# Performance work log

Hardware: AMD Instinct MI355X
Metric: run time of the kernel (lower is better)

Reference implementation:

```python
import jax, jax.numpy as jnp
import numpy as np

T, B, L, S = 2048, 64, 32, 256
NEG = -1e30  # effective -inf, safe under logaddexp


def setup_inputs() -> dict:
    key = jax.random.key(0)
    k1, k2, k3 = jax.random.split(key, 3)
    inputs = jax.random.normal(k1, (T, B, L), dtype=jnp.float32)
    targets = jax.random.randint(k2, (B, S), 0, L)
    input_lengths = jnp.full((B,), T, dtype=jnp.int32)
    target_lengths = jnp.full((B,), S, dtype=jnp.int32)
    # learned transition matrix (param of ASGLoss); small random for a non-trivial test
    transition = 0.1 * jax.random.normal(k3, (L, L), dtype=jnp.float32)
    return {"transition": transition, "inputs": inputs, "targets": targets,
            "input_lengths": input_lengths, "target_lengths": target_lengths}


def _fcc_scores(transition, inputs, input_lengths):
    # Fully-connected forward: alpha_t[i] = emit_t[i] + logsumexp_j(alpha_{t-1}[j] + trans[i,j])
    alpha0 = inputs[0]  # [B, L]

    def step(alpha, emit):
        new = emit + jax.nn.logsumexp(alpha[:, None, :] + transition[None, :, :], axis=2)
        return new, new

    _, rest = jax.lax.scan(step, alpha0, inputs[1:])
    alphas = jnp.concatenate([alpha0[None], rest], axis=0)  # [T, B, L]
    b = jnp.arange(inputs.shape[1])
    # causal DP: alpha at t = len-1 is exactly the score for that length
    return jax.nn.logsumexp(alphas[input_lengths - 1, b], axis=-1)  # [B]


def _fac_scores(transition, inputs, targets, input_lengths, target_lengths):
    # Force-aligned forward over target positions s:
    # alpha_t[s] = emit_t[tgt_s] + logaddexp(alpha_{t-1}[s] + trans[tgt_s,tgt_s],
    #                                        alpha_{t-1}[s-1] + trans[tgt_s,tgt_{s-1}])
    Tn, Bn, _ = inputs.shape
    Sn = targets.shape[1]
    # gathered emissions for target labels: [T, B, S]
    emit = jnp.take_along_axis(inputs, jnp.broadcast_to(targets[None], (Tn, Bn, Sn)), axis=2)
    self_tr = transition[targets, targets]                       # [B, S] stay score
    prev = jnp.concatenate([targets[:, :1], targets[:, :-1]], 1)
    move_tr = transition[targets, prev]                          # [B, S] move score (s=0 unused)

    alpha0 = jnp.where((jnp.arange(Sn) == 0)[None, :], emit[0], NEG)  # only s=0 at t=0

    def step(alpha, e):
        stay = alpha + self_tr
        moved = jnp.concatenate(
            [jnp.full_like(alpha[:, :1], NEG), alpha[:, :-1] + move_tr[:, 1:]], axis=1)
        new = e + jnp.logaddexp(stay, moved)
        return new, new

    _, rest = jax.lax.scan(step, alpha0, emit[1:])
    alphas = jnp.concatenate([alpha0[None], rest], axis=0)  # [T, B, S]
    b = jnp.arange(Bn)
    return alphas[input_lengths - 1, b, target_lengths - 1]  # [B]


def reference(transition, inputs, targets, input_lengths, target_lengths):
    # original clamps targets to input length; S <= T here so it's a no-op
    fcc = _fcc_scores(transition, inputs, input_lengths)
    fac = _fac_scores(transition, inputs, targets, input_lengths, target_lengths)
    result = fcc - fac  # [B]
    return result.mean()  # reduction='mean'
```

## Files before the change

kernel.cpp:

```cpp
#include <hip/hip_runtime.h>
#include <math.h>

static constexpr int TB = 64;
static constexpr int LL = 32;
static constexpr int SS = 256;
static constexpr int STRIDE_T = TB * LL;

static constexpr int OF_FWD  = 0;
static constexpr int OF_BWD  = 33;
static constexpr int OF_FACF = 2178;
static constexpr int OF_FACB = 2498;
static constexpr int WSB     = 2818;

#define LN2F 0.69314718055994530942f
#define NEGF (-1e30f)

#define BARX() { asm volatile("s_waitcnt lgkmcnt(0)" ::: "memory"); \
                 __builtin_amdgcn_s_barrier(); \
                 asm volatile("" ::: "memory"); }

template<int CTL>
__device__ __forceinline__ float dpp_f(float x, float oldv) {
  return __int_as_float(__builtin_amdgcn_update_dpp(
      __float_as_int(oldv), __float_as_int(x), CTL, 0xF, 0xF, false));
}
template<int M>
__device__ __forceinline__ int rot_i(int x) {
  return __builtin_amdgcn_update_dpp(0, x, 0x120 + M, 0xF, 0xF, false);
}

typedef unsigned uint2v __attribute__((ext_vector_type(2)));
__device__ __forceinline__ float xsum16(float x) {
  uint2v r = __builtin_amdgcn_permlane16_swap(__float_as_uint(x), __float_as_uint(x), false, false);
  return __uint_as_float(r.x) + __uint_as_float(r.y);
}
__device__ __forceinline__ float xsum32(float x) {
  uint2v r = __builtin_amdgcn_permlane32_swap(__float_as_uint(x), __float_as_uint(x), false, false);
  return __uint_as_float(r.x) + __uint_as_float(r.y);
}
__device__ __forceinline__ float bperm(int addr, float src) {
  return __int_as_float(__builtin_amdgcn_ds_bpermute(addr, __float_as_int(src)));
}

template<int M>
struct Calib {
  __device__ static __forceinline__ void run(const float* trans, int lam, int i, float* Ec) {
    Ec[M] = __expf(trans[i * LL + rot_i<M>(lam)]);
    Calib<M + 1>::run(trans, lam, i, Ec);
  }
};
template<> struct Calib<16> {
  __device__ static __forceinline__ void run(const float*, int, int, float*) {}
};
template<int M>
struct CalibT {
  __device__ static __forceinline__ void run(const float* trans, int lam, int i, float* Ec) {
    Ec[M] = __expf(trans[rot_i<M>(lam) * LL + i]);
    CalibT<M + 1>::run(trans, lam, i, Ec);
  }
};
template<> struct CalibT<16> {
  __device__ static __forceinline__ void run(const float*, int, int, float*) {}
};

#define ROT_MUL(DST, SRC, COEF, ROT) \
  asm("v_mul_f32_dpp %0, %1, %2 row_ror:" #ROT " row_mask:0xf bank_mask:0xf" \
      : "=v"(DST) : "v"(SRC), "v"(COEF))
#define ROT_FMAC(ACC, SRC, COEF, ROT) \
  asm("v_fmac_f32_dpp %0, %1, %2 row_ror:" #ROT " row_mask:0xf bank_mask:0xf" \
      : "+v"(ACC) : "v"(SRC), "v"(COEF))

#define STEP16(EC) { \
  float a0 = EC[0] * A, a1, a2, a3; \
  ROT_MUL(a1, A, EC[1], 1); ROT_MUL(a2, A, EC[2], 2); ROT_MUL(a3, A, EC[3], 3); \
  ROT_FMAC(a0, A, EC[4], 4);  ROT_FMAC(a1, A, EC[5], 5); \
  ROT_FMAC(a2, A, EC[6], 6);  ROT_FMAC(a3, A, EC[7], 7); \
  ROT_FMAC(a0, A, EC[8], 8);  ROT_FMAC(a1, A, EC[9], 9); \
  ROT_FMAC(a2, A, EC[10], 10); ROT_FMAC(a3, A, EC[11], 11); \
  ROT_FMAC(a0, A, EC[12], 12); ROT_FMAC(a1, A, EC[13], 13); \
  ROT_FMAC(a2, A, EC[14], 14); ROT_FMAC(a3, A, EC[15], 15); \
  part = (a0 + a1) + (a2 + a3); }


#define FCC_RENORM() { \
  unsigned uu = (unsigned)__builtin_amdgcn_readfirstlane((int)__float_as_uint(A)); \
  int ex = (int)((uu >> 23) & 255) - 127; \
  A = ldexpf(A, -ex); Kt += ex; }

#define FCC_CONSUME8(PB) { \
  float eb[8]; \
  _Pragma("unroll") for (int q = 0; q < 8; ++q) eb[q] = sE[PB][q][(q & 1) ? lam1 : lam2]; \
  { float part; STEP16(Ec1); A = eb[0] * xsum16(part); } \
  { float part; STEP16(Ec2); A = eb[1] * xsum32(part); } \
  { float part; STEP16(Ec1); A = eb[2] * xsum16(part); } \
  { float part; STEP16(Ec2); A = eb[3] * xsum32(part); } \
  { float part; STEP16(Ec1); A = eb[4] * xsum16(part); } \
  { float part; STEP16(Ec2); A = eb[5] * xsum32(part); } \
  { float part; STEP16(Ec1); A = eb[6] * xsum16(part); } \
  { float part; STEP16(Ec2); A = eb[7] * xsum32(part); } \
  FCC_RENORM(); }

#define FCC_TAIL(PB, CNT) { \
  float eb[8]; \
  _Pragma("unroll") for (int q = 0; q < 8; ++q) eb[q] = sE[PB][q][(q & 1) ? lam1 : lam2]; \
  _Pragma("unroll") for (int q = 0; q < 8; ++q) { \
    if (q >= (CNT)) break; \
    if ((q & 1) == 0) { float part; STEP16(Ec1); A = eb[q] * xsum16(part); } \
    else              { float part; STEP16(Ec2); A = eb[q] * xsum32(part); } } }

#define FCC_BWDCON8(PB) { \
  float eb[8]; \
  _Pragma("unroll") for (int q = 0; q < 8; ++q) eb[q] = sE[PB][q][(q & 1) ? lam1 : lam2]; \
  { A *= eb[7]; float part; STEP16(E1T); A = xsum16(part); } \
  { A *= eb[6]; float part; STEP16(E2T); A = xsum32(part); } \
  { A *= eb[5]; float part; STEP16(E1T); A = xsum16(part); } \
  { A *= eb[4]; float part; STEP16(E2T); A = xsum32(part); } \
  { A *= eb[3]; float part; STEP16(E1T); A = xsum16(part); } \
  { A *= eb[2]; float part; STEP16(E2T); A = xsum32(part); } \
  { A *= eb[1]; float part; STEP16(E1T); A = xsum16(part); } \
  { A *= eb[0]; float part; STEP16(E2T); A = xsum32(part); } \
  FCC_RENORM(); }


#define FAC_STEP(E0, E1, E2, E3) { \
  float ap = dpp_f<0x138>(A3, 0.f);  \
  float n0 = (E0) * fmaf(MV0b,  ap, ST[0] * A0); \
  float n1 = (E1) * fmaf(MVl[1], A0, ST[1] * A1); \
  float n2 = (E2) * fmaf(MVl[2], A1, ST[2] * A2); \
  float n3 = (E3) * fmaf(MVl[3], A2, ST[3] * A3); \
  A0 = n0; A1 = n1; A2 = n2; A3 = n3; }

#define FAC_BOUNDARY() { \
  float maxA = fmaxf(fmaxf(A0, A1), fmaxf(A2, A3)); \
  if (maxA > 0.f) { \
    int ex = (int)((__float_as_uint(maxA) >> 23) & 255) - 127; \
    A0 = ldexpf(A0, -ex); A1 = ldexpf(A1, -ex); \
    A2 = ldexpf(A2, -ex); A3 = ldexpf(A3, -ex); \
    m += (float)ex; \
  } \
  float mp = dpp_f<0x138>(m, NEGF); m = (m == NEGF) ? mp : m; \
  mp = dpp_f<0x138>(m, NEGF);       m = (m == NEGF) ? mp : m; \
  mp = dpp_f<0x138>(m, NEGF); \
  float dlt = fminf(mp - m, 50.0f); \
  float Sin = exp2f(dlt); \
  MV0b = MVl[0] * Sin; }

#define FACF_CON8(PB) { \
  float4 Er[8]; \
  _Pragma("unroll") for (int r = 0; r < 8; ++r) Er[r] = sF[PB][r][l]; \
  _Pragma("unroll") for (int r = 0; r < 8; ++r) \
    FAC_STEP(Er[r].x, Er[r].y, Er[r].z, Er[r].w); \
  FAC_BOUNDARY(); }

#define FACF_TAIL(PB, CNT) { \
  float4 Er[8]; \
  _Pragma("unroll") for (int r = 0; r < 8; ++r) Er[r] = sF[PB][r][l]; \
  _Pragma("unroll") for (int r = 0; r < 8; ++r) { \
    if (r >= (CNT)) break; \
    FAC_STEP(Er[r].x, Er[r].y, Er[r].z, Er[r].w); } }

#define FACB_BOUNDARY() { \
  float maxA = fmaxf(fmaxf(A0, A1), fmaxf(A2, A3)); \
  if (maxA > 0.f) { \
    int ex = (int)((__float_as_uint(maxA) >> 23) & 255) - 127; \
    A0 = ldexpf(A0, -ex); A1 = ldexpf(A1, -ex); \
    A2 = ldexpf(A2, -ex); A3 = ldexpf(A3, -ex); \
    m += (float)ex; \
  } \
  float mp = dpp_f<0x130>(m, NEGF); m = (m == NEGF) ? mp : m; \
  mp = dpp_f<0x130>(m, NEGF);       m = (m == NEGF) ? mp : m; \
  mp = dpp_f<0x130>(m, NEGF); \
  float dlt = fminf(mp - m, 50.0f); \
  MVn3b = MVn[3] * exp2f(dlt); }

#define FACB_CON8(PB) { \
  float4 Er[8]; \
  _Pragma("unroll") for (int r = 0; r < 8; ++r) Er[r] = sF[PB][r][l]; \
  _Pragma("unroll") for (int i = 0; i < 8; ++i) { \
    const int q = 7 - i; \
    float en3 = dpp_f<0x130>(Er[q].x, 0.f);  \
    float an  = dpp_f<0x130>(A0, 0.f); \
    float n0 = fmaf(Er[q].y * MVn[0], A1, Er[q].x * ST[0] * A0); \
    float n1 = fmaf(Er[q].z * MVn[1], A2, Er[q].y * ST[1] * A1); \
    float n2 = fmaf(Er[q].w * MVn[2], A3, Er[q].z * ST[2] * A2); \
    float n3 = fmaf(en3 * MVn3b,      an, Er[q].w * ST[3] * A3); \
    A0 = n0; A1 = n1; A2 = n2; A3 = n3; } \
  FACB_BOUNDARY(); }


#define HLD(Q, K) ({ \
  int tt_ = (isfwd ? (1 + 8 * (Q)) : (lenm1 - 8 * (Q) - 7)) + 2 * (K) + rowoff; \
  tt_ = tt_ < 0 ? 0 : (tt_ > lenm1 ? lenm1 : tt_); \
  gpl[(size_t)tt_ * STRIDE_T]; })

#define PROD_FCC(PB, KK, RV) { sE[PB][2 * (KK) + rowoff][lam1] = __expf(RV); }

#define PROD_FAC(PB, KK, RV) { \
  float e_ = __expf(RV); \
  float4 E0_, E1_; \
  E0_.x = bperm(adA[0], e_); E0_.y = bperm(adA[1], e_); \
  E0_.z = bperm(adA[2], e_); E0_.w = bperm(adA[3], e_); \
  E1_.x = bperm(adB[0], e_); E1_.y = bperm(adB[1], e_); \
  E1_.z = bperm(adB[2], e_); E1_.w = bperm(adB[3], e_); \
  sF[PB][2 * (KK)][l]     = E0_; \
  sF[PB][2 * (KK) + 1][l] = E1_; }


extern "C" __global__ __launch_bounds__(192, 1)
void asg_main(const float* __restrict__ trans, const float* __restrict__ inputs,
              const int* __restrict__ targets, const int* __restrict__ ilen,
              const int* __restrict__ tlen, float* __restrict__ ws) {
  const int tid = (int)threadIdx.x;
  const int w = tid >> 6;
  const int l = tid & 63;
  const int lam1 = l & 31;
  const int lam2 = (l & 15) | ((l >> 5) << 4);
  const int rowoff = l >> 5;

  const int role = (int)blockIdx.x >> 6;
  const int b    = (int)blockIdx.x & 63;

  const int len = ilen[b];
  const int lenm1 = len - 1;
  const int Lsteps = lenm1;
  const int nb = (Lsteps / 2) & ~7;
  const int nf = Lsteps - nb;
  const bool isfwd = (role == 0) || (role == 2);
  const int nsteps = isfwd ? nf : nb;
  const int nph = (nsteps + 7) >> 3;

  const float* gpl = inputs + (size_t)b * LL + lam1;
  float* P = ws + (size_t)b * WSB;

  __shared__ float  sE[2][8][32];
  __shared__ float4 sF[2][8][64];

  if (w == 0) {
    __builtin_amdgcn_s_setprio(1);

    if (role == 0) {
      float Ec1[16], Ec2[16];
      Ec1[0] = __expf(trans[lam2 * LL + lam1]);
      Ec2[0] = __expf(trans[lam1 * LL + lam2]);
      Calib<1>::run(trans, lam1, lam2, Ec1);
      Calib<1>::run(trans, lam2, lam1, Ec2);
      float A = __expf(inputs[(size_t)b * LL + lam1]);
      int Kt = 0;
      for (int p = 0; p < nph; p += 2) {
        BARX();
        { const int rem = nsteps - 8 * p;
          if (rem >= 8) { FCC_CONSUME8(0); } else { FCC_TAIL(0, rem); } }
        BARX();
        if (p + 1 < nph) {
          const int rem = nsteps - 8 * (p + 1);
          if (rem >= 8) { FCC_CONSUME8(1); } else { FCC_TAIL(1, rem); }
        }
      }
      const int par = nsteps & 1;
      const int idx = par ? lam2 : lam1;
      const bool wr = par ? ((l & 16) == 0) : (l < 32);
      if (wr) P[OF_FWD + idx] = A;
      if (l == 0) P[OF_FWD + 32] = (float)Kt;

    } else if (role == 1) {
      float E1T[16], E2T[16];
      E1T[0] = __expf(trans[lam1 * LL + lam2]);
      E2T[0] = __expf(trans[lam2 * LL + lam1]);
      CalibT<1>::run(trans, lam1, lam2, E1T);
      CalibT<1>::run(trans, lam2, lam1, E2T);
      float A = 1.f;
      int Kt = 0;
      for (int p = 0; p < nph; p += 2) {
        BARX();
        FCC_BWDCON8(0);
        BARX();
        if (p + 1 < nph) { FCC_BWDCON8(1); }
      }
      if (l < 32) P[OF_BWD + lam1] = A;
      if (l == 0) P[OF_BWD + 32] = (float)Kt;

    } else if (role == 2) {
      int tg[4];
      #pragma unroll
      for (int q = 0; q < 4; ++q) tg[q] = targets[b * SS + 4 * l + q];
      float ST[4], MVl[4];
      #pragma unroll
      for (int q = 0; q < 4; ++q) ST[q] = __expf(trans[tg[q] * LL + tg[q]]);
      MVl[0] = (l == 0) ? 0.f : __expf(trans[tg[0] * LL + targets[b * SS + 4 * l - 1]]);
      #pragma unroll
      for (int q = 1; q < 4; ++q) MVl[q] = __expf(trans[tg[q] * LL + tg[q - 1]]);

      float A0 = (l == 0) ? __expf(inputs[(size_t)b * LL + tg[0]]) : 0.f;
      float A1 = 0.f, A2 = 0.f, A3 = 0.f;
      float m  = (l == 0) ? 0.f : NEGF;
      float MV0b;
      FAC_BOUNDARY();

      for (int p = 0; p < nph; p += 2) {
        BARX();
        { const int rem = nsteps - 8 * p;
          if (rem >= 8) { FACF_CON8(0); } else { FACF_TAIL(0, rem); } }
        BARX();
        if (p + 1 < nph) {
          const int rem = nsteps - 8 * (p + 1);
          if (rem >= 8) { FACF_CON8(1); } else { FACF_TAIL(1, rem); }
        }
      }
      P[OF_FACF + 4 * l + 0] = A0;
      P[OF_FACF + 4 * l + 1] = A1;
      P[OF_FACF + 4 * l + 2] = A2;
      P[OF_FACF + 4 * l + 3] = A3;
      P[OF_FACF + 256 + l]   = m;

    } else {
      const int tl = tlen[b];
      const int fs = tl - 1;
      int tg[4];
      #pragma unroll
      for (int q = 0; q < 4; ++q) tg[q] = targets[b * SS + 4 * l + q];
      float ST[4], MVn[4];
      #pragma unroll
      for (int q = 0; q < 4; ++q) ST[q] = __expf(trans[tg[q] * LL + tg[q]]);
      MVn[0] = __expf(trans[tg[1] * LL + tg[0]]);
      MVn[1] = __expf(trans[tg[2] * LL + tg[1]]);
      MVn[2] = __expf(trans[tg[3] * LL + tg[2]]);
      int tgn3 = (l < 63) ? targets[b * SS + 4 * l + 4] : 0;
      MVn[3] = (l < 63) ? __expf(trans[tgn3 * LL + tg[3]]) : 0.f;

      float A0 = (4 * l + 0 == fs) ? 1.f : 0.f;
      float A1 = (4 * l + 1 == fs) ? 1.f : 0.f;
      float A2 = (4 * l + 2 == fs) ? 1.f : 0.f;
      float A3 = (4 * l + 3 == fs) ? 1.f : 0.f;
      float m  = (l == (fs >> 2)) ? 0.f : NEGF;
      float MVn3b;
      FACB_BOUNDARY();

      for (int p = 0; p < nph; p += 2) {
        BARX();
        FACB_CON8(0);
        BARX();
        if (p + 1 < nph) { FACB_CON8(1); }
      }
      P[OF_FACB + 4 * l + 0] = A0;
      P[OF_FACB + 4 * l + 1] = A1;
      P[OF_FACB + 4 * l + 2] = A2;
      P[OF_FACB + 4 * l + 3] = A3;
      P[OF_FACB + 256 + l]   = m;
    }

  } else {
    const int kh = 2 * (w - 1);
    const bool fac = (role >= 2);
    int adA[4] = {0, 0, 0, 0}, adB[4] = {0, 0, 0, 0};
    if (fac) {
      #pragma unroll
      for (int j = 0; j < 4; ++j) {
        int tg = targets[b * SS + 4 * l + j];
        adA[j] = tg * 4; adB[j] = adA[j] + 128;
      }
    }
    if (nph > 0) {
      float p0a = HLD(0, kh), p0b = HLD(0, kh + 1);
      float sAa = HLD(1, kh), sAb = HLD(1, kh + 1);
      float sBa = HLD(2, kh), sBb = HLD(2, kh + 1);
      if (fac) { PROD_FAC(0, kh, p0a); PROD_FAC(0, kh + 1, p0b); }
      else     { PROD_FCC(0, kh, p0a); PROD_FCC(0, kh + 1, p0b); }

      for (int p = 0; p < nph; p += 2) {
        BARX();
        if (p + 1 < nph) {
          if (fac) { PROD_FAC(1, kh, sAa); PROD_FAC(1, kh + 1, sAb); }
          else     { PROD_FCC(1, kh, sAa); PROD_FCC(1, kh + 1, sAb); }
          sAa = HLD(p + 3, kh); sAb = HLD(p + 3, kh + 1);
        }
        BARX();
        if (p + 2 < nph) {
          if (fac) { PROD_FAC(0, kh, sBa); PROD_FAC(0, kh + 1, sBb); }
          else     { PROD_FCC(0, kh, sBa); PROD_FCC(0, kh + 1, sBb); }
          sBa = HLD(p + 4, kh); sBb = HLD(p + 4, kh + 1);
        }
      }
    }
  }
}


extern "C" __global__ __launch_bounds__(1024)
void asg_combine(const float* __restrict__ ws, float* __restrict__ out) {
  __shared__ float sd[TB];
  const int tid = (int)threadIdx.x;
  const int w = tid >> 6, l = tid & 63;

  for (int k = 0; k < 4; ++k) {
    const int b = w * 4 + k;
    const float* P = ws + (size_t)b * WSB;

    float al = (l < 32) ? P[OF_FWD + l] : 0.f;
    float vv = (l < 32) ? P[OF_BWD + l] : 0.f;
    float s = al * vv;
    #pragma unroll
    for (int mm = 1; mm < 64; mm <<= 1) s += __shfl_xor(s, mm);
    float fcc = __logf(s) + (P[OF_FWD + 32] + P[OF_BWD + 32]) * LN2F;

    float pa = P[OF_FACF + 4 * l + 0] * P[OF_FACB + 4 * l + 0]
             + P[OF_FACF + 4 * l + 1] * P[OF_FACB + 4 * l + 1]
             + P[OF_FACF + 4 * l + 2] * P[OF_FACB + 4 * l + 2]
             + P[OF_FACF + 4 * l + 3] * P[OF_FACB + 4 * l + 3];
    float sc = P[OF_FACF + 256 + l] + P[OF_FACB + 256 + l];
    float Ms = sc;
    #pragma unroll
    for (int mm = 1; mm < 64; mm <<= 1) Ms = fmaxf(Ms, __shfl_xor(Ms, mm));
    float pp = pa * exp2f(sc - Ms);
    #pragma unroll
    for (int mm = 1; mm < 64; mm <<= 1) pp += __shfl_xor(pp, mm);
    float fac = __logf(pp) + Ms * LN2F;

    if (l == 0) sd[b] = fcc - fac;
  }
  __syncthreads();
  if (tid < TB) {
    float d = sd[tid];
    #pragma unroll
    for (int mm = 1; mm < 64; mm <<= 1) d += __shfl_xor(d, mm);
    if (tid == 0) out[0] = d * (1.0f / TB);
  }
}


extern "C" void kernel_launch(void* const* d_in, const int* in_sizes, int n_in,
                              void* d_out, int out_size, void* d_ws, size_t ws_size,
                              hipStream_t stream) {
  const float* trans   = (const float*)d_in[0];
  const float* inputs  = (const float*)d_in[1];
  const int*   targets = (const int*)d_in[2];
  const int*   ilen    = (const int*)d_in[3];
  const int*   tlen    = (const int*)d_in[4];
  float* out = (float*)d_out;
  float* ws  = (float*)d_ws;

  asg_main<<<dim3(4 * TB), dim3(192), 0, stream>>>(trans, inputs, targets, ilen, tlen, ws);
  asg_combine<<<dim3(1), dim3(1024), 0, stream>>>(ws, out);
}
```

Before: 82.51 us.

## Split FCC time recursion into eight chunks and prefold FAC transition coefficients

The fully-connected forward/backward scan is cut into NCH=8 time chunks per batch. Each interior chunk runs both a forward pass from a unit vector and a backward pass from a unit vector, and the combine kernel stitches the chunks together with dot products and normalising logs. This shortens the serial dependency chain of the FCC scan, which was the critical path, but launches many more blocks and does more total work. The FAC producers now prefold the stay and move transition factors into separate shared-memory arrays, removing multiplies from the consumer's recurrence. The STEP16 accumulation is also widened to eight partial sums to shorten the FMA chain.

```diff
diff --git a/kernel.cpp b/kernel.cpp
--- a/kernel.cpp
+++ b/kernel.cpp
@@ -6,11 +6,14 @@
 static constexpr int SS = 256;
 static constexpr int STRIDE_T = TB * LL;
 
-static constexpr int OF_FWD  = 0;
-static constexpr int OF_BWD  = 33;
-static constexpr int OF_FACF = 2178;
-static constexpr int OF_FACB = 2498;
-static constexpr int WSB     = 2818;
+static constexpr int NCH = 8;
+static constexpr int NI  = NCH - 2;
+static constexpr int NSCAN = 2 + 2 * NI;
+
+static constexpr int OF_FCC  = 0;
+static constexpr int OF_FACF = 512;
+static constexpr int OF_FACB = 832;
+static constexpr int WSB     = 1152;
 
 #define LN2F 0.69314718055994530942f
 #define NEGF (-1e30f)
@@ -71,15 +74,15 @@
       : "+v"(ACC) : "v"(SRC), "v"(COEF))
 
 #define STEP16(EC) { \
-  float a0 = EC[0] * A, a1, a2, a3; \
+  float a0 = EC[0] * A, a1, a2, a3, a4, a5, a6, a7; \
   ROT_MUL(a1, A, EC[1], 1); ROT_MUL(a2, A, EC[2], 2); ROT_MUL(a3, A, EC[3], 3); \
-  ROT_FMAC(a0, A, EC[4], 4);  ROT_FMAC(a1, A, EC[5], 5); \
-  ROT_FMAC(a2, A, EC[6], 6);  ROT_FMAC(a3, A, EC[7], 7); \
-  ROT_FMAC(a0, A, EC[8], 8);  ROT_FMAC(a1, A, EC[9], 9); \
+  ROT_MUL(a4, A, EC[4], 4); ROT_MUL(a5, A, EC[5], 5); ROT_MUL(a6, A, EC[6], 6); \
+  ROT_MUL(a7, A, EC[7], 7); \
+  ROT_FMAC(a0, A, EC[8], 8);   ROT_FMAC(a1, A, EC[9], 9); \
   ROT_FMAC(a2, A, EC[10], 10); ROT_FMAC(a3, A, EC[11], 11); \
-  ROT_FMAC(a0, A, EC[12], 12); ROT_FMAC(a1, A, EC[13], 13); \
-  ROT_FMAC(a2, A, EC[14], 14); ROT_FMAC(a3, A, EC[15], 15); \
-  part = (a0 + a1) + (a2 + a3); }
+  ROT_FMAC(a4, A, EC[12], 12); ROT_FMAC(a5, A, EC[13], 13); \
+  ROT_FMAC(a6, A, EC[14], 14); ROT_FMAC(a7, A, EC[15], 15); \
+  part = ((a0 + a1) + (a2 + a3)) + ((a4 + a5) + (a6 + a7)); }
 
 
 #define FCC_RENORM() { \
@@ -100,7 +103,7 @@
   { float part; STEP16(Ec2); A = eb[7] * xsum32(part); } \
   FCC_RENORM(); }
 
-#define FCC_TAIL(PB, CNT) { \
+#define FCC_TAIL8(PB, CNT) { \
   float eb[8]; \
   _Pragma("unroll") for (int q = 0; q < 8; ++q) eb[q] = sE[PB][q][(q & 1) ? lam1 : lam2]; \
   _Pragma("unroll") for (int q = 0; q < 8; ++q) { \
@@ -122,15 +125,7 @@
   FCC_RENORM(); }
 
 
-#define FAC_STEP(E0, E1, E2, E3) { \
-  float ap = dpp_f<0x138>(A3, 0.f);  \
-  float n0 = (E0) * fmaf(MV0b,  ap, ST[0] * A0); \
-  float n1 = (E1) * fmaf(MVl[1], A0, ST[1] * A1); \
-  float n2 = (E2) * fmaf(MVl[2], A1, ST[2] * A2); \
-  float n3 = (E3) * fmaf(MVl[3], A2, ST[3] * A3); \
-  A0 = n0; A1 = n1; A2 = n2; A3 = n3; }
-
-#define FAC_BOUNDARY() { \
+#define FAC_BOUNDARY_S() { \
   float maxA = fmaxf(fmaxf(A0, A1), fmaxf(A2, A3)); \
   if (maxA > 0.f) { \
     int ex = (int)((__float_as_uint(maxA) >> 23) & 255) - 127; \
@@ -142,24 +137,35 @@
   mp = dpp_f<0x138>(m, NEGF);       m = (m == NEGF) ? mp : m; \
   mp = dpp_f<0x138>(m, NEGF); \
   float dlt = fminf(mp - m, 50.0f); \
-  float Sin = exp2f(dlt); \
-  MV0b = MVl[0] * Sin; }
+  Sin = exp2f(dlt); }
 
 #define FACF_CON8(PB) { \
-  float4 Er[8]; \
-  _Pragma("unroll") for (int r = 0; r < 8; ++r) Er[r] = sF[PB][r][l]; \
-  _Pragma("unroll") for (int r = 0; r < 8; ++r) \
-    FAC_STEP(Er[r].x, Er[r].y, Er[r].z, Er[r].w); \
-  FAC_BOUNDARY(); }
-
-#define FACF_TAIL(PB, CNT) { \
-  float4 Er[8]; \
-  _Pragma("unroll") for (int r = 0; r < 8; ++r) Er[r] = sF[PB][r][l]; \
+  float4 Sr[8], Mr[8]; \
+  _Pragma("unroll") for (int r = 0; r < 8; ++r) { Sr[r] = sFa[PB][r][l]; Mr[r] = sFb[PB][r][l]; } \
+  _Pragma("unroll") for (int r = 0; r < 8; ++r) { \
+    float t0 = Mr[r].x * Sin; \
+    float ap = dpp_f<0x138>(A3, 0.f);  \
+    float n0 = fmaf(t0,      ap, Sr[r].x * A0); \
+    float n1 = fmaf(Mr[r].y, A0, Sr[r].y * A1); \
+    float n2 = fmaf(Mr[r].z, A1, Sr[r].z * A2); \
+    float n3 = fmaf(Mr[r].w, A2, Sr[r].w * A3); \
+    A0 = n0; A1 = n1; A2 = n2; A3 = n3; } \
+  FAC_BOUNDARY_S(); }
+
+#define FACF_TAIL8(PB, CNT) { \
+  float4 Sr[8], Mr[8]; \
+  _Pragma("unroll") for (int r = 0; r < 8; ++r) { Sr[r] = sFa[PB][r][l]; Mr[r] = sFb[PB][r][l]; } \
   _Pragma("unroll") for (int r = 0; r < 8; ++r) { \
     if (r >= (CNT)) break; \
-    FAC_STEP(Er[r].x, Er[r].y, Er[r].z, Er[r].w); } }
-
-#define FACB_BOUNDARY() { \
+    float t0 = Mr[r].x * Sin; \
+    float ap = dpp_f<0x138>(A3, 0.f); \
+    float n0 = fmaf(t0,      ap, Sr[r].x * A0); \
+    float n1 = fmaf(Mr[r].y, A0, Sr[r].y * A1); \
+    float n2 = fmaf(Mr[r].z, A1, Sr[r].z * A2); \
+    float n3 = fmaf(Mr[r].w, A2, Sr[r].w * A3); \
+    A0 = n0; A1 = n1; A2 = n2; A3 = n3; } }
+
+#define FACB_BOUNDARY_S() { \
   float maxA = fmaxf(fmaxf(A0, A1), fmaxf(A2, A3)); \
   if (maxA > 0.f) { \
     int ex = (int)((__float_as_uint(maxA) >> 23) & 255) - 127; \
@@ -171,39 +177,64 @@
   mp = dpp_f<0x130>(m, NEGF);       m = (m == NEGF) ? mp : m; \
   mp = dpp_f<0x130>(m, NEGF); \
   float dlt = fminf(mp - m, 50.0f); \
-  MVn3b = MVn[3] * exp2f(dlt); }
+  Sb = exp2f(dlt); }
 
 #define FACB_CON8(PB) { \
-  float4 Er[8]; \
-  _Pragma("unroll") for (int r = 0; r < 8; ++r) Er[r] = sF[PB][r][l]; \
+  float4 Sr[8], Mr[8]; \
+  _Pragma("unroll") for (int r = 0; r < 8; ++r) { Sr[r] = sFa[PB][r][l]; Mr[r] = sFb[PB][r][l]; } \
   _Pragma("unroll") for (int i = 0; i < 8; ++i) { \
     const int q = 7 - i; \
-    float en3 = dpp_f<0x130>(Er[q].x, 0.f);  \
-    float an  = dpp_f<0x130>(A0, 0.f); \
-    float n0 = fmaf(Er[q].y * MVn[0], A1, Er[q].x * ST[0] * A0); \
-    float n1 = fmaf(Er[q].z * MVn[1], A2, Er[q].y * ST[1] * A1); \
-    float n2 = fmaf(Er[q].w * MVn[2], A3, Er[q].z * ST[2] * A2); \
-    float n3 = fmaf(en3 * MVn3b,      an, Er[q].w * ST[3] * A3); \
+    float t3 = Mr[q].w * Sb; \
+    float an = dpp_f<0x130>(A0, 0.f);  \
+    float n0 = fmaf(Mr[q].x, A1, Sr[q].x * A0); \
+    float n1 = fmaf(Mr[q].y, A2, Sr[q].y * A1); \
+    float n2 = fmaf(Mr[q].z, A3, Sr[q].z * A2); \
+    float n3 = fmaf(t3,      an, Sr[q].w * A3); \
     A0 = n0; A1 = n1; A2 = n2; A3 = n3; } \
-  FACB_BOUNDARY(); }
-
-
-#define HLD(Q, K) ({ \
-  int tt_ = (isfwd ? (1 + 8 * (Q)) : (lenm1 - 8 * (Q) - 7)) + 2 * (K) + rowoff; \
+  FACB_BOUNDARY_S(); }
+
+
+#define HLDF(Q, K) ({ \
+  int tt_ = t0 + 8 * (Q) + 2 * (K) + rowoff; \
+  tt_ = tt_ > lenm1 ? lenm1 : tt_; \
+  gpl[(size_t)tt_ * STRIDE_T]; })
+#define HLDB(Q, K) ({ \
+  int tt_ = thi - 8 * (Q) - 7 + 2 * (K) + rowoff; \
   tt_ = tt_ < 0 ? 0 : (tt_ > lenm1 ? lenm1 : tt_); \
   gpl[(size_t)tt_ * STRIDE_T]; })
+#define HLD2(Q, K) ( isfwd ? HLDF(Q, K) : HLDB(Q, K) )
 
 #define PROD_FCC(PB, KK, RV) { sE[PB][2 * (KK) + rowoff][lam1] = __expf(RV); }
 
-#define PROD_FAC(PB, KK, RV) { \
+#define PRODF_FWD(PB, KK, RV) { \
   float e_ = __expf(RV); \
-  float4 E0_, E1_; \
-  E0_.x = bperm(adA[0], e_); E0_.y = bperm(adA[1], e_); \
-  E0_.z = bperm(adA[2], e_); E0_.w = bperm(adA[3], e_); \
-  E1_.x = bperm(adB[0], e_); E1_.y = bperm(adB[1], e_); \
-  E1_.z = bperm(adB[2], e_); E1_.w = bperm(adB[3], e_); \
-  sF[PB][2 * (KK)][l]     = E0_; \
-  sF[PB][2 * (KK) + 1][l] = E1_; }
+  float c0 = bperm(adA[0], e_), c1 = bperm(adA[1], e_); \
+  float c2 = bperm(adA[2], e_), c3 = bperm(adA[3], e_); \
+  float4 sa, sb; \
+  sa.x = c0 * ST[0]; sa.y = c1 * ST[1]; sa.z = c2 * ST[2]; sa.w = c3 * ST[3]; \
+  sb.x = c0 * CM[0]; sb.y = c1 * CM[1]; sb.z = c2 * CM[2]; sb.w = c3 * CM[3]; \
+  sFa[PB][2 * (KK)][l] = sa; sFb[PB][2 * (KK)][l] = sb; \
+  float d0 = bperm(adB[0], e_), d1 = bperm(adB[1], e_); \
+  float d2 = bperm(adB[2], e_), d3 = bperm(adB[3], e_); \
+  sa.x = d0 * ST[0]; sa.y = d1 * ST[1]; sa.z = d2 * ST[2]; sa.w = d3 * ST[3]; \
+  sb.x = d0 * CM[0]; sb.y = d1 * CM[1]; sb.z = d2 * CM[2]; sb.w = d3 * CM[3]; \
+  sFa[PB][2 * (KK) + 1][l] = sa; sFb[PB][2 * (KK) + 1][l] = sb; }
+
+#define PRODF_BWD(PB, KK, RV) { \
+  float e_ = __expf(RV); \
+  float c0 = bperm(adA[0], e_), c1 = bperm(adA[1], e_); \
+  float c2 = bperm(adA[2], e_), c3 = bperm(adA[3], e_); \
+  float cn = bperm(adN, e_); \
+  float4 sa, sb; \
+  sa.x = c0 * ST[0]; sa.y = c1 * ST[1]; sa.z = c2 * ST[2]; sa.w = c3 * ST[3]; \
+  sb.x = c1 * CM[0]; sb.y = c2 * CM[1]; sb.z = c3 * CM[2]; sb.w = cn * CM[3]; \
+  sFa[PB][2 * (KK)][l] = sa; sFb[PB][2 * (KK)][l] = sb; \
+  float d0 = bperm(adB[0], e_), d1 = bperm(adB[1], e_); \
+  float d2 = bperm(adB[2], e_), d3 = bperm(adB[3], e_); \
+  float dn = bperm(adNB, e_); \
+  sa.x = d0 * ST[0]; sa.y = d1 * ST[1]; sa.z = d2 * ST[2]; sa.w = d3 * ST[3]; \
+  sb.x = d1 * CM[0]; sb.y = d2 * CM[1]; sb.z = d3 * CM[2]; sb.w = dn * CM[3]; \
+  sFa[PB][2 * (KK) + 1][l] = sa; sFb[PB][2 * (KK) + 1][l] = sb; }
 
 
 extern "C" __global__ __launch_bounds__(192, 1)
@@ -216,94 +247,150 @@
   const int lam1 = l & 31;
   const int lam2 = (l & 15) | ((l >> 5) << 4);
   const int rowoff = l >> 5;
-
-  const int role = (int)blockIdx.x >> 6;
-  const int b    = (int)blockIdx.x & 63;
+  const int bid = (int)blockIdx.x;
+
+  __shared__ float  sE[2][8][32];
+  __shared__ float4 sFa[2][8][64];
+  __shared__ float4 sFb[2][8][64];
+
+  if (bid < NSCAN * TB) {
+    const int s = bid >> 6;
+    const int b = bid & 63;
+    const int len = ilen[b];
+    const int lenm1 = len - 1;
+    const int Lsteps = lenm1;
+    const int L  = (Lsteps / NCH) & ~7;
+    const int n0 = Lsteps - (NCH - 1) * L;
+
+    bool isfwd; int t0 = 1, thi = lenm1, nsteps, outslot;
+    if (s == 0)      { isfwd = true;  t0 = 1; nsteps = n0; outslot = 0; }
+    else if (s == 1) { isfwd = false; thi = lenm1; nsteps = L; outslot = 1; }
+    else {
+      const int j = s >> 1;
+      if ((s & 1) == 0) { isfwd = true;  t0 = n0 + (j - 1) * L + 1; nsteps = L; outslot = 2 * j; }
+      else              { isfwd = false; thi = n0 + j * L;          nsteps = L; outslot = 2 * j + 1; }
+    }
+    const int nph = (nsteps + 7) >> 3;
+    const float* gpl = inputs + (size_t)b * LL + lam1;
+    float* P = ws + (size_t)b * WSB + OF_FCC + outslot * 33;
+
+    if (w == 0) {
+      __builtin_amdgcn_s_setprio(1);
+      if (isfwd) {
+        float Ec1[16], Ec2[16];
+        Ec1[0] = __expf(trans[lam2 * LL + lam1]);
+        Ec2[0] = __expf(trans[lam1 * LL + lam2]);
+        Calib<1>::run(trans, lam1, lam2, Ec1);
+        Calib<1>::run(trans, lam2, lam1, Ec2);
+        float A = (s == 0) ? __expf(inputs[(size_t)b * LL + lam1]) : 1.f;
+        int Kt = 0;
+        for (int p = 0; p < nph; p += 2) {
+          BARX();
+          { const int rem = nsteps - 8 * p;
+            if (rem >= 8) { FCC_CONSUME8(0); } else { FCC_TAIL8(0, rem); } }
+          BARX();
+          if (p + 1 < nph) {
+            const int rem = nsteps - 8 * (p + 1);
+            if (rem >= 8) { FCC_CONSUME8(1); } else { FCC_TAIL8(1, rem); }
+          }
+        }
+        const int par = nsteps & 1;
+        const int idx = par ? lam2 : lam1;
+        const bool wr = par ? ((l & 16) == 0) : (l < 32);
+        if (wr) P[idx] = A;
+        if (l == 0) P[32] = (float)Kt;
+      } else {
+        float E1T[16], E2T[16];
+        E1T[0] = __expf(trans[lam1 * LL + lam2]);
+        E2T[0] = __expf(trans[lam2 * LL + lam1]);
+        CalibT<1>::run(trans, lam1, lam2, E1T);
+        CalibT<1>::run(trans, lam2, lam1, E2T);
+        float A = 1.f;
+        int Kt = 0;
+        for (int p = 0; p < nph; p += 2) {
+          BARX();
+          FCC_BWDCON8(0);
+          BARX();
+          if (p + 1 < nph) { FCC_BWDCON8(1); }
+        }
+        if (l < 32) P[lam1] = A;
+        if (l == 0) P[32] = (float)Kt;
+      }
+    } else if (w == 1) {
+      float R1[4], R2[4], R3[4];
+      #pragma unroll
+      for (int k = 0; k < 4; ++k) R1[k] = HLD2(0, k);
+      #pragma unroll
+      for (int k = 0; k < 4; ++k) R2[k] = HLD2(1, k);
+      #pragma unroll
+      for (int k = 0; k < 4; ++k) R3[k] = HLD2(2, k);
+      #pragma unroll
+      for (int k = 0; k < 4; ++k) PROD_FCC(0, k, R1[k]);
+      #pragma unroll
+      for (int k = 0; k < 4; ++k) { R1[k] = R2[k]; R2[k] = R3[k]; R3[k] = HLD2(3, k); }
+      for (int p = 0; p < nph; p += 2) {
+        BARX();
+        if (p + 1 < nph) {
+          float N[4];
+          #pragma unroll
+          for (int k = 0; k < 4; ++k) N[k] = HLD2(p + 4, k);
+          #pragma unroll
+          for (int k = 0; k < 4; ++k) PROD_FCC(1, k, R1[k]);
+          #pragma unroll
+          for (int k = 0; k < 4; ++k) { R1[k] = R2[k]; R2[k] = R3[k]; R3[k] = N[k]; }
+        }
+        BARX();
+        if (p + 2 < nph) {
+          float N[4];
+          #pragma unroll
+          for (int k = 0; k < 4; ++k) N[k] = HLD2(p + 5, k);
+          #pragma unroll
+          for (int k = 0; k < 4; ++k) PROD_FCC(0, k, R1[k]);
+          #pragma unroll
+          for (int k = 0; k < 4; ++k) { R1[k] = R2[k]; R2[k] = R3[k]; R3[k] = N[k]; }
+        }
+      }
+    } else {
+      const int I = (nph + 1) >> 1;
+      for (int i = 0; i < I; ++i) { BARX(); BARX(); }
+    }
+    return;
+  }
+
+  const int rid  = bid - NSCAN * TB;
+  const int role = rid >> 6;
+  const int b    = rid & 63;
 
   const int len = ilen[b];
   const int lenm1 = len - 1;
   const int Lsteps = lenm1;
-  const int nb = (Lsteps / 2) & ~7;
-  const int nf = Lsteps - nb;
-  const bool isfwd = (role == 0) || (role == 2);
-  const int nsteps = isfwd ? nf : nb;
+  const int nbf = (Lsteps / 2) & ~7;
+  const int nff = Lsteps - nbf;
+  const bool isfwd = (role == 0);
+  const int t0 = 1, thi = lenm1;
+  const int nsteps = isfwd ? nff : nbf;
   const int nph = (nsteps + 7) >> 3;
 
   const float* gpl = inputs + (size_t)b * LL + lam1;
   float* P = ws + (size_t)b * WSB;
 
-  __shared__ float  sE[2][8][32];
-  __shared__ float4 sF[2][8][64];
-
   if (w == 0) {
     __builtin_amdgcn_s_setprio(1);
-
-    if (role == 0) {
-      float Ec1[16], Ec2[16];
-      Ec1[0] = __expf(trans[lam2 * LL + lam1]);
-      Ec2[0] = __expf(trans[lam1 * LL + lam2]);
-      Calib<1>::run(trans, lam1, lam2, Ec1);
-      Calib<1>::run(trans, lam2, lam1, Ec2);
-      float A = __expf(inputs[(size_t)b * LL + lam1]);
-      int Kt = 0;
+    if (isfwd) {
+      const int tg0 = targets[b * SS + 4 * l];
+      float A0 = (l == 0) ? __expf(inputs[(size_t)b * LL + tg0]) : 0.f;
+      float A1 = 0.f, A2 = 0.f, A3 = 0.f;
+      float m  = (l == 0) ? 0.f : NEGF;
+      float Sin;
+      FAC_BOUNDARY_S();
       for (int p = 0; p < nph; p += 2) {
         BARX();
         { const int rem = nsteps - 8 * p;
-          if (rem >= 8) { FCC_CONSUME8(0); } else { FCC_TAIL(0, rem); } }
+          if (rem >= 8) { FACF_CON8(0); } else { FACF_TAIL8(0, rem); } }
         BARX();
         if (p + 1 < nph) {
           const int rem = nsteps - 8 * (p + 1);
-          if (rem >= 8) { FCC_CONSUME8(1); } else { FCC_TAIL(1, rem); }
-        }
-      }
-      const int par = nsteps & 1;
-      const int idx = par ? lam2 : lam1;
-      const bool wr = par ? ((l & 16) == 0) : (l < 32);
-      if (wr) P[OF_FWD + idx] = A;
-      if (l == 0) P[OF_FWD + 32] = (float)Kt;
-
-    } else if (role == 1) {
-      float E1T[16], E2T[16];
-      E1T[0] = __expf(trans[lam1 * LL + lam2]);
-      E2T[0] = __expf(trans[lam2 * LL + lam1]);
-      CalibT<1>::run(trans, lam1, lam2, E1T);
-      CalibT<1>::run(trans, lam2, lam1, E2T);
-      float A = 1.f;
-      int Kt = 0;
-      for (int p = 0; p < nph; p += 2) {
-        BARX();
-        FCC_BWDCON8(0);
-        BARX();
-        if (p + 1 < nph) { FCC_BWDCON8(1); }
-      }
-      if (l < 32) P[OF_BWD + lam1] = A;
-      if (l == 0) P[OF_BWD + 32] = (float)Kt;
-
-    } else if (role == 2) {
-      int tg[4];
-      #pragma unroll
-      for (int q = 0; q < 4; ++q) tg[q] = targets[b * SS + 4 * l + q];
-      float ST[4], MVl[4];
-      #pragma unroll
-      for (int q = 0; q < 4; ++q) ST[q] = __expf(trans[tg[q] * LL + tg[q]]);
-      MVl[0] = (l == 0) ? 0.f : __expf(trans[tg[0] * LL + targets[b * SS + 4 * l - 1]]);
-      #pragma unroll
-      for (int q = 1; q < 4; ++q) MVl[q] = __expf(trans[tg[q] * LL + tg[q - 1]]);
-
-      float A0 = (l == 0) ? __expf(inputs[(size_t)b * LL + tg[0]]) : 0.f;
-      float A1 = 0.f, A2 = 0.f, A3 = 0.f;
-      float m  = (l == 0) ? 0.f : NEGF;
-      float MV0b;
-      FAC_BOUNDARY();
-
-      for (int p = 0; p < nph; p += 2) {
-        BARX();
-        { const int rem = nsteps - 8 * p;
-          if (rem >= 8) { FACF_CON8(0); } else { FACF_TAIL(0, rem); } }
-        BARX();
-        if (p + 1 < nph) {
-          const int rem = nsteps - 8 * (p + 1);
-          if (rem >= 8) { FACF_CON8(1); } else { FACF_TAIL(1, rem); }
+          if (rem >= 8) { FACF_CON8(1); } else { FACF_TAIL8(1, rem); }
         }
       }
       P[OF_FACF + 4 * l + 0] = A0;
@@ -311,30 +398,16 @@
       P[OF_FACF + 4 * l + 2] = A2;
       P[OF_FACF + 4 * l + 3] = A3;
       P[OF_FACF + 256 + l]   = m;
-
     } else {
       const int tl = tlen[b];
       const int fs = tl - 1;
-      int tg[4];
-      #pragma unroll
-      for (int q = 0; q < 4; ++q) tg[q] = targets[b * SS + 4 * l + q];
-      float ST[4], MVn[4];
-      #pragma unroll
-      for (int q = 0; q < 4; ++q) ST[q] = __expf(trans[tg[q] * LL + tg[q]]);
-      MVn[0] = __expf(trans[tg[1] * LL + tg[0]]);
-      MVn[1] = __expf(trans[tg[2] * LL + tg[1]]);
-      MVn[2] = __expf(trans[tg[3] * LL + tg[2]]);
-      int tgn3 = (l < 63) ? targets[b * SS + 4 * l + 4] : 0;
-      MVn[3] = (l < 63) ? __expf(trans[tgn3 * LL + tg[3]]) : 0.f;
-
       float A0 = (4 * l + 0 == fs) ? 1.f : 0.f;
       float A1 = (4 * l + 1 == fs) ? 1.f : 0.f;
       float A2 = (4 * l + 2 == fs) ? 1.f : 0.f;
       float A3 = (4 * l + 3 == fs) ? 1.f : 0.f;
       float m  = (l == (fs >> 2)) ? 0.f : NEGF;
-      float MVn3b;
-      FACB_BOUNDARY();
-
+      float Sb;
+      FACB_BOUNDARY_S();
       for (int p = 0; p < nph; p += 2) {
         BARX();
         FACB_CON8(0);
@@ -347,38 +420,52 @@
       P[OF_FACB + 4 * l + 3] = A3;
       P[OF_FACB + 256 + l]   = m;
     }
-
   } else {
     const int kh = 2 * (w - 1);
-    const bool fac = (role >= 2);
-    int adA[4] = {0, 0, 0, 0}, adB[4] = {0, 0, 0, 0};
-    if (fac) {
-      #pragma unroll
-      for (int j = 0; j < 4; ++j) {
-        int tg = targets[b * SS + 4 * l + j];
-        adA[j] = tg * 4; adB[j] = adA[j] + 128;
+    int tg[4];
+    #pragma unroll
+    for (int q = 0; q < 4; ++q) tg[q] = targets[b * SS + 4 * l + q];
+    float ST[4], CM[4];
+    #pragma unroll
+    for (int q = 0; q < 4; ++q) ST[q] = __expf(trans[tg[q] * LL + tg[q]]);
+    int adA[4], adB[4], adN = 0, adNB = 0;
+    #pragma unroll
+    for (int j = 0; j < 4; ++j) { adA[j] = tg[j] * 4; adB[j] = adA[j] + 128; }
+    if (isfwd) {
+      CM[0] = (l == 0) ? 0.f : __expf(trans[tg[0] * LL + targets[b * SS + 4 * l - 1]]);
+      #pragma unroll
+      for (int q = 1; q < 4; ++q) CM[q] = __expf(trans[tg[q] * LL + tg[q - 1]]);
+    } else {
+      CM[0] = __expf(trans[tg[1] * LL + tg[0]]);
+      CM[1] = __expf(trans[tg[2] * LL + tg[1]]);
+      CM[2] = __expf(trans[tg[3] * LL + tg[2]]);
+      int tgn3 = (l < 63) ? targets[b * SS + 4 * l + 4] : 0;
+      CM[3] = (l < 63) ? __expf(trans[tgn3 * LL + tg[3]]) : 0.f;
+      adN = tgn3 * 4; adNB = adN + 128;
+    }
+
+    float R1a = HLD2(0, kh), R1b = HLD2(0, kh + 1);
+    float R2a = HLD2(1, kh), R2b = HLD2(1, kh + 1);
+    float R3a = HLD2(2, kh), R3b = HLD2(2, kh + 1);
+    if (isfwd) { PRODF_FWD(0, kh, R1a); PRODF_FWD(0, kh + 1, R1b); }
+    else       { PRODF_BWD(0, kh, R1a); PRODF_BWD(0, kh + 1, R1b); }
+    R1a = R2a; R1b = R2b; R2a = R3a; R2b = R3b;
+    R3a = HLD2(3, kh); R3b = HLD2(3, kh + 1);
+
+    for (int p = 0; p < nph; p += 2) {
+      BARX();
+      if (p + 1 < nph) {
+        float Na = HLD2(p + 4, kh), Nb = HLD2(p + 4, kh + 1);
+        if (isfwd) { PRODF_FWD(1, kh, R1a); PRODF_FWD(1, kh + 1, R1b); }
+        else       { PRODF_BWD(1, kh, R1a); PRODF_BWD(1, kh + 1, R1b); }
+        R1a = R2a; R1b = R2b; R2a = R3a; R2b = R3b; R3a = Na; R3b = Nb;
       }
-    }
-    if (nph > 0) {
-      float p0a = HLD(0, kh), p0b = HLD(0, kh + 1);
-      float sAa = HLD(1, kh), sAb = HLD(1, kh + 1);
-      float sBa = HLD(2, kh), sBb = HLD(2, kh + 1);
-      if (fac) { PROD_FAC(0, kh, p0a); PROD_FAC(0, kh + 1, p0b); }
-      else     { PROD_FCC(0, kh, p0a); PROD_FCC(0, kh + 1, p0b); }
-
-      for (int p = 0; p < nph; p += 2) {
-        BARX();
-        if (p + 1 < nph) {
-          if (fac) { PROD_FAC(1, kh, sAa); PROD_FAC(1, kh + 1, sAb); }
-          else     { PROD_FCC(1, kh, sAa); PROD_FCC(1, kh + 1, sAb); }
-          sAa = HLD(p + 3, kh); sAb = HLD(p + 3, kh + 1);
-        }
-        BARX();
-        if (p + 2 < nph) {
-          if (fac) { PROD_FAC(0, kh, sBa); PROD_FAC(0, kh + 1, sBb); }
-          else     { PROD_FCC(0, kh, sBa); PROD_FCC(0, kh + 1, sBb); }
-          sBa = HLD(p + 4, kh); sBb = HLD(p + 4, kh + 1);
-        }
+      BARX();
+      if (p + 2 < nph) {
+        float Na = HLD2(p + 5, kh), Nb = HLD2(p + 5, kh + 1);
+        if (isfwd) { PRODF_FWD(0, kh, R1a); PRODF_FWD(0, kh + 1, R1b); }
+        else       { PRODF_BWD(0, kh, R1a); PRODF_BWD(0, kh + 1, R1b); }
+        R1a = R2a; R1b = R2b; R2a = R3a; R2b = R3b; R3a = Na; R3b = Nb;
       }
     }
   }
@@ -395,12 +482,28 @@
     const int b = w * 4 + k;
     const float* P = ws + (size_t)b * WSB;
 
-    float al = (l < 32) ? P[OF_FWD + l] : 0.f;
-    float vv = (l < 32) ? P[OF_BWD + l] : 0.f;
-    float s = al * vv;
-    #pragma unroll
-    for (int mm = 1; mm < 64; mm <<= 1) s += __shfl_xor(s, mm);
-    float fcc = __logf(s) + (P[OF_FWD + 32] + P[OF_BWD + 32]) * LN2F;
+    float acc = 0.f;
+    float Ksum = P[OF_FCC + 0 * 33 + 32];
+    #pragma unroll
+    for (int j = 0; j <= NI; ++j) {
+      const int qs = (j == NI) ? 1 : (2 * j + 3);
+      const int ps = (j == 0) ? 0 : (2 * j);
+      float qv = (l < 32) ? P[OF_FCC + qs * 33 + l] : 0.f;
+      float pv = (l < 32) ? P[OF_FCC + ps * 33 + l] : 0.f;
+      float d = qv * pv;
+      #pragma unroll
+      for (int mm = 1; mm < 64; mm <<= 1) d += __shfl_xor(d, mm);
+      acc += __logf(d);
+      Ksum += P[OF_FCC + qs * 33 + 32];
+    }
+    #pragma unroll
+    for (int j = 1; j <= NI; ++j) {
+      float pv = (l < 32) ? P[OF_FCC + 2 * j * 33 + l] : 0.f;
+      #pragma unroll
+      for (int mm = 1; mm < 64; mm <<= 1) pv += __shfl_xor(pv, mm);
+      acc -= __logf(pv);
+    }
+    float fcc = acc + Ksum * LN2F;
 
     float pa = P[OF_FACF + 4 * l + 0] * P[OF_FACB + 4 * l + 0]
              + P[OF_FACF + 4 * l + 1] * P[OF_FACB + 4 * l + 1]
@@ -438,6 +541,7 @@
   float* out = (float*)d_out;
   float* ws  = (float*)d_ws;
 
-  asg_main<<<dim3(4 * TB), dim3(192), 0, stream>>>(trans, inputs, targets, ilen, tlen, ws);
+  asg_main<<<dim3((NSCAN + 2) * TB), dim3(192), 0, stream>>>(
+      trans, inputs, targets, ilen, tlen, ws);
   asg_combine<<<dim3(1), dim3(1024), 0, stream>>>(ws, out);
 }
```

Result: slower. 97.63 us (+18.3%).
